# Optimization experiments

Measured on AMD Instinct MI355X. Metric: run time of the kernel, lower is better.

The kernel has to match this reference:

```python
import jax, jax.numpy as jnp
import numpy as np

Z, Y, X = 32, 480, 480          # sparse voxel grid (LiDAR-scale)
N = 200_000                     # active voxels
C_IN, C_OUT = 64, 64
EPS = 1e-5


def _subm_conv(f, nbr, w):
    """Submanifold sparse conv as gather-matmul-accumulate.
    f: [N, Cin]; nbr: [N, K] neighbor row ids, pad index == N for missing;
    w: [K, Cin, Cout]."""
    f_pad = jnp.concatenate([f, jnp.zeros((1, f.shape[1]), f.dtype)], axis=0)
    g = f_pad[nbr]                       # [N, K, Cin] gathered neighbor features
    return jnp.einsum('nkc,kco->no', g, w)


def _bn(x, gamma, beta):
    # BatchNorm1d in training mode: batch stats over the N dimension
    m = x.mean(axis=0)
    v = x.var(axis=0)
    return (x - m) * jax.lax.rsqrt(v + EPS) * gamma + beta


def setup_inputs() -> dict:
    rng = np.random.default_rng(0)
    ids = rng.choice(Z * Y * X, size=N, replace=False)
    lookup = np.full(Z * Y * X, -1, dtype=np.int64)
    lookup[ids] = np.arange(N)
    z = ids // (Y * X)
    y = (ids // X) % Y
    x = ids % X

    def nbr_table(offsets):
        cols = []
        for dz, dy, dx in offsets:
            zz, yy, xx = z + dz, y + dy, x + dx
            ok = (zz >= 0) & (zz < Z) & (yy >= 0) & (yy < Y) & (xx >= 0) & (xx < X)
            lin = np.clip((zz * Y + yy) * X + xx, 0, Z * Y * X - 1)
            idx = np.where(ok, lookup[lin], -1)
            cols.append(np.where(idx >= 0, idx, N))   # pad index N -> zero row
        return jnp.asarray(np.stack(cols, axis=1).astype(np.int32))

    off13 = [(0, dy, dx) for dy in (-1, 0, 1) for dx in (-1, 0, 1)]  # kernel (1,3,3)
    off31 = [(dz, 0, dx) for dz in (-1, 0, 1) for dx in (-1, 0, 1)]  # kernel (3,1,3)

    key = jax.random.key(0)
    ks = jax.random.split(key, 5)
    s = 0.05
    ones = jnp.ones((C_OUT,), jnp.float32)
    zeros = jnp.zeros((C_OUT,), jnp.float32)
    return {
        'features': jax.random.normal(ks[0], (N, C_IN), jnp.float32),
        'w1':   jax.random.normal(ks[1], (9, C_IN, C_OUT), jnp.float32) * s,
        'w1_2': jax.random.normal(ks[2], (9, C_OUT, C_OUT), jnp.float32) * s,
        'w2':   jax.random.normal(ks[3], (9, C_IN, C_OUT), jnp.float32) * s,
        'w3':   jax.random.normal(ks[4], (9, C_OUT, C_OUT), jnp.float32) * s,
        'g0': ones, 'b0': zeros, 'g0_2': ones, 'b0_2': zeros,
        'g1': ones, 'b1': zeros, 'g2': ones, 'b2': zeros,
        'nbr13': nbr_table(off13),
        'nbr31': nbr_table(off31),
    }


def reference(features, w1, w1_2, w2, w3, g0, b0, g0_2, b0_2, g1, b1, g2, b2,
              nbr13, nbr31):
    # shortcut branch: conv1x3 -> LeakyReLU -> BN -> conv3x1 -> LeakyReLU -> BN
    sc = _subm_conv(features, nbr13, w1)
    sc = _bn(jax.nn.leaky_relu(sc), g0, b0)
    sc = _subm_conv(sc, nbr31, w1_2)
    sc = _bn(jax.nn.leaky_relu(sc), g0_2, b0_2)
    # main branch: conv3x1 -> LeakyReLU -> BN -> conv1x3 -> LeakyReLU -> BN
    r = _subm_conv(features, nbr31, w2)
    r = _bn(jax.nn.leaky_relu(r), g1, b1)
    r = _subm_conv(r, nbr13, w3)
    r = _bn(jax.nn.leaky_relu(r), g2, b2)
    return r + sc
```

## Files before the change

### kernel.cpp

```cpp
#include <hip/hip_runtime.h>

#define NVOX 200000
#define TM 128
#define NBLK 1563
#define NBLK3 521
#define NREP 32
#define STG 4224

typedef unsigned short u16;
typedef unsigned int u32;
typedef __bf16 bf16x8 __attribute__((ext_vector_type(8)));
typedef float f32x16 __attribute__((ext_vector_type(16)));

__device__ __forceinline__ float bf2f(u16 h) { return __uint_as_float(((u32)h) << 16); }
__device__ __forceinline__ u16 f2bf(float x) {
  u32 u = __float_as_uint(x);
  u32 r = u + 0x7fffu + ((u >> 16) & 1u);
  return (u16)(r >> 16);
}
__device__ __forceinline__ uint4 cvt8(uint4 a, uint4 b) {
  const float* fa = (const float*)&a;
  const float* fb = (const float*)&b;
  uint4 r;
  u16* q = (u16*)&r;
#pragma unroll
  for (int j = 0; j < 4; ++j) { q[j] = f2bf(fa[j]); q[4 + j] = f2bf(fb[j]); }
  return r;
}

template <int PHASE>
__global__ __launch_bounds__(256, 2)
void conv_fused(const u16* __restrict__ inA, const u16* __restrict__ inB,
                const int* __restrict__ nbrA, const int* __restrict__ nbrB,
                const u16* __restrict__ wfA, const u16* __restrict__ wfB,
                const u16* __restrict__ zrow,
                void* yA, void* yB, float* __restrict__ stA, float* __restrict__ stB) {
  __shared__ float sred[4][128];

  const int tid = threadIdx.x;
  const int bid = blockIdx.x;
  const bool hB = (bid >= NBLK3);
  const int blk = hB ? bid - NBLK3 : bid;
  const u16* f = hB ? inB : inA;
  const int* nbr = hB ? nbrB : nbrA;
  const u16* wf = hB ? wfB : wfA;
  float* st = hB ? stB : stA;

  const int wv = tid >> 6;
  const int lane = tid & 63;
  const int lrow = lane & 31;
  const int lq = lane >> 5;
  const int wbase = blk * 384 + wv * 96;
  const int gr0 = wbase + lrow;
  const int gr1 = gr0 + 32;
  const int gr2 = gr0 + 64;

  constexpr bool FOLDED = (PHASE == 1);
  constexpr int KSTRIDE = FOLDED ? 5120 : 4096;

  f32x16 zz = {0.f, 0.f, 0.f, 0.f, 0.f, 0.f, 0.f, 0.f,
               0.f, 0.f, 0.f, 0.f, 0.f, 0.f, 0.f, 0.f};
  f32x16 a00 = zz, a01 = zz, a10 = zz, a11 = zz, a20 = zz, a21 = zz;

  int ic0 = (gr0 < NVOX) ? nbr[gr0 * 9] : NVOX;
  int ic1 = (gr1 < NVOX) ? nbr[gr1 * 9] : NVOX;
  int ic2 = (gr2 < NVOX) ? nbr[gr2 * 9] : NVOX;

  uint4 X[4], Y[4];

  for (int k = 0; k < 9; ++k) {
    const u16* wb = wf + k * KSTRIDE;
    bf16x8 wreg[8];
#pragma unroll
    for (int fi = 0; fi < 8; ++fi)
      wreg[fi] = __builtin_bit_cast(bf16x8, *(const uint4*)(wb + fi * 512 + lane * 8));
    bf16x8 wrb0, wrb1;
    if constexpr (FOLDED) {
      wrb0 = __builtin_bit_cast(bf16x8, *(const uint4*)(wb + 8 * 512 + lane * 8));
      wrb1 = __builtin_bit_cast(bf16x8, *(const uint4*)(wb + 9 * 512 + lane * 8));
    }
    int in0 = NVOX, in1 = NVOX, in2 = NVOX;
    if (k < 8) {
      in0 = (gr0 < NVOX) ? nbr[gr0 * 9 + k + 1] : NVOX;
      in1 = (gr1 < NVOX) ? nbr[gr1 * 9 + k + 1] : NVOX;
      in2 = (gr2 < NVOX) ? nbr[gr2 * 9 + k + 1] : NVOX;
    }

    const bool l0 = (k == 4) || (__ballot(ic0 < NVOX) != 0ull);
    const bool l1 = (k == 4) || (__ballot(ic1 < NVOX) != 0ull);
    const bool l2 = (k == 4) || (__ballot(ic2 < NVOX) != 0ull);

    auto G = [&](uint4 (&d)[4], int id) {
      const u16* p = (id < NVOX) ? (f + (size_t)id * 64) : zrow;
      p += lq * 8;
      d[0] = *(const uint4*)(p);
      d[1] = *(const uint4*)(p + 16);
      d[2] = *(const uint4*)(p + 32);
      d[3] = *(const uint4*)(p + 48);
    };
    auto MMA = [&](f32x16& c0, f32x16& c1, const uint4 (&s)[4], int id) {
#pragma unroll
      for (int ksi = 0; ksi < 4; ++ksi) {
        bf16x8 a = __builtin_bit_cast(bf16x8, s[ksi]);
        c0 = __builtin_amdgcn_mfma_f32_32x32x16_bf16(a, wreg[ksi * 2], c0, 0, 0, 0);
        c1 = __builtin_amdgcn_mfma_f32_32x32x16_bf16(a, wreg[ksi * 2 + 1], c1, 0, 0, 0);
      }
      if constexpr (FOLDED) {
        uint4 a4 = make_uint4(0u, 0u, 0u, 0u);
        if (lq == 0 && id < NVOX) ((u16*)&a4)[0] = 0x3F80u;
        bf16x8 a = __builtin_bit_cast(bf16x8, a4);
        c0 = __builtin_amdgcn_mfma_f32_32x32x16_bf16(a, wrb0, c0, 0, 0, 0);
        c1 = __builtin_amdgcn_mfma_f32_32x32x16_bf16(a, wrb1, c1, 0, 0, 0);
      }
    };

    if (l0) G(X, ic0);
    if (l1) G(Y, ic1);
    if (l0) MMA(a00, a01, X, ic0);
    if (l2) G(X, ic2);
    if (l1) MMA(a10, a11, Y, ic1);
    if (l2) MMA(a20, a21, X, ic2);

    ic0 = in0; ic1 = in1; ic2 = in2;
  }

  const bool f32out = (PHASE == 1) && !hB;
  float* yf = (float*)yA;
  u16* yb = (u16*)(hB ? yB : yA);
  float s0 = 0.f, q0 = 0.f, s1 = 0.f, q1 = 0.f;

  auto EPI = [&](const f32x16& c0, const f32x16& c1, int g) {
    const int row0 = wbase + g * 32 + 4 * lq;
#pragma unroll
    for (int r = 0; r < 16; ++r) {
      float v = c0[r]; v = v > 0.f ? v : 0.01f * v;
      float w = c1[r]; w = w > 0.f ? w : 0.01f * w;
      s0 += v; q0 += v * v; s1 += w; q1 += w * w;
      const int row = row0 + (r & 3) + 8 * (r >> 2);
      if (row < NVOX) {
        if (f32out) {
          yf[(size_t)row * 64 + lrow] = v;
          yf[(size_t)row * 64 + 32 + lrow] = w;
        } else {
          yb[(size_t)row * 64 + lrow] = f2bf(v);
          yb[(size_t)row * 64 + 32 + lrow] = f2bf(w);
        }
      }
    }
  };
  EPI(a00, a01, 0); EPI(a10, a11, 1); EPI(a20, a21, 2);

  s0 += __shfl_xor(s0, 32); q0 += __shfl_xor(q0, 32);
  s1 += __shfl_xor(s1, 32); q1 += __shfl_xor(q1, 32);
  if (lq == 0) {
    sred[wv][lrow] = s0; sred[wv][32 + lrow] = s1;
    sred[wv][64 + lrow] = q0; sred[wv][96 + lrow] = q1;
  }
  __syncthreads();
  if (tid < 128) {
    int which = tid >> 6, c = tid & 63;
    float v = sred[0][which * 64 + c] + sred[1][which * 64 + c] +
              sred[2][which * 64 + c] + sred[3][which * 64 + c];
    atomicAdd(&st[(bid & (NREP - 1)) * 128 + which * 64 + c], v);
  }
}

template <bool IN_F32, bool FOLDED, int MODE>
__global__ __launch_bounds__(256, 4)
void conv_k(const void* __restrict__ fv, const int* __restrict__ nbr,
            const u16* __restrict__ wf, void* yv, float* __restrict__ st,
            float* io, const float* __restrict__ affD,
            const float* __restrict__ affB) {
  __shared__ __align__(16) float fb[128 * 68];
  __shared__ float sred[4][128];

  const int tid = threadIdx.x;
  const int wv = tid >> 6;
  const int lane = tid & 63;
  const int lrow = lane & 31;
  const int lq = lane >> 5;
  const int base = blockIdx.x * TM;
  const int gr = base + wv * 32 + lrow;

  int ids[9];
#pragma unroll
  for (int j = 0; j < 9; ++j) ids[j] = (gr < NVOX) ? nbr[gr * 9 + j] : NVOX;

  f32x16 acc0 = {0.f, 0.f, 0.f, 0.f, 0.f, 0.f, 0.f, 0.f,
                 0.f, 0.f, 0.f, 0.f, 0.f, 0.f, 0.f, 0.f};
  f32x16 acc1 = acc0;
  constexpr int KSTRIDE = FOLDED ? 5120 : 4096;

#pragma unroll
  for (int k = 0; k < 9; ++k) {
    if (k != 4) {
      if (__ballot(ids[k] < NVOX) == 0ull) continue;
    }
    const int id = ids[k];
    const bool ok = id < NVOX;
    uint4 af[4];
    if constexpr (IN_F32) {
      const float* p = (const float*)fv + (size_t)id * 64 + lq * 8;
#pragma unroll
      for (int ksi = 0; ksi < 4; ++ksi) {
        uint4 v0 = make_uint4(0u, 0u, 0u, 0u), v1 = v0;
        if (ok) { v0 = *(const uint4*)(p + ksi * 16); v1 = *(const uint4*)(p + ksi * 16 + 4); }
        af[ksi] = cvt8(v0, v1);
      }
    } else {
      const u16* p = (const u16*)fv + (size_t)id * 64 + lq * 8;
#pragma unroll
      for (int ksi = 0; ksi < 4; ++ksi) {
        uint4 v = make_uint4(0u, 0u, 0u, 0u);
        if (ok) v = *(const uint4*)(p + ksi * 16);
        af[ksi] = v;
      }
    }
    const u16* wb = wf + k * KSTRIDE;
#pragma unroll
    for (int ksi = 0; ksi < 4; ++ksi) {
      bf16x8 a = __builtin_bit_cast(bf16x8, af[ksi]);
      bf16x8 b0 = __builtin_bit_cast(bf16x8, *(const uint4*)(wb + (ksi * 2) * 512 + lane * 8));
      bf16x8 b1 = __builtin_bit_cast(bf16x8, *(const uint4*)(wb + (ksi * 2 + 1) * 512 + lane * 8));
      acc0 = __builtin_amdgcn_mfma_f32_32x32x16_bf16(a, b0, acc0, 0, 0, 0);
      acc1 = __builtin_amdgcn_mfma_f32_32x32x16_bf16(a, b1, acc1, 0, 0, 0);
    }
    if constexpr (FOLDED) {
      uint4 a4 = make_uint4(0u, 0u, 0u, 0u);
      if (lq == 0 && ok) ((u16*)&a4)[0] = 0x3F80u;
      bf16x8 a = __builtin_bit_cast(bf16x8, a4);
      bf16x8 b0 = __builtin_bit_cast(bf16x8, *(const uint4*)(wb + 8 * 512 + lane * 8));
      bf16x8 b1 = __builtin_bit_cast(bf16x8, *(const uint4*)(wb + 9 * 512 + lane * 8));
      acc0 = __builtin_amdgcn_mfma_f32_32x32x16_bf16(a, b0, acc0, 0, 0, 0);
      acc1 = __builtin_amdgcn_mfma_f32_32x32x16_bf16(a, b1, acc1, 0, 0, 0);
    }
  }

  const int cc0 = lrow, cc1 = 32 + lrow;
  float aD0 = 0.f, aD1 = 0.f, hD0 = 0.f, hD1 = 0.f;
  if constexpr (MODE == 2) {
    aD0 = affD[cc0]; hD0 = affD[64 + cc0];
    aD1 = affD[cc1]; hD1 = affD[64 + cc1];
  }
  float s0 = 0.f, q0 = 0.f, s1 = 0.f, q1 = 0.f;
  float vout[2][16];
#pragma unroll
  for (int r = 0; r < 16; ++r) {
    float v = acc0[r]; v = v > 0.f ? v : 0.01f * v;
    s0 += v; q0 += v * v; vout[0][r] = v;
    float w = acc1[r]; w = w > 0.f ? w : 0.01f * w;
    s1 += w; q1 += w * w; vout[1][r] = w;
  }
  if constexpr (MODE != 2) {
    s0 += __shfl_xor(s0, 32); q0 += __shfl_xor(q0, 32);
    s1 += __shfl_xor(s1, 32); q1 += __shfl_xor(q1, 32);
    if (lq == 0) {
      sred[wv][lrow] = s0; sred[wv][32 + lrow] = s1;
      sred[wv][64 + lrow] = q0; sred[wv][96 + lrow] = q1;
    }
  }
  if constexpr (MODE == 0) {
    u16* bb = (u16*)fb;
#pragma unroll
    for (int r = 0; r < 16; ++r) {
      int rowD = 32 * wv + (r & 3) + 8 * (r >> 2) + 4 * lq;
      bb[rowD * 72 + cc0] = f2bf(vout[0][r]);
      bb[rowD * 72 + cc1] = f2bf(vout[1][r]);
    }
  } else if constexpr (MODE == 2 || MODE == 3) {
#pragma unroll
    for (int r = 0; r < 16; ++r) {
      int rowD = 32 * wv + (r & 3) + 8 * (r >> 2) + 4 * lq;
      float v0 = vout[0][r], v1 = vout[1][r];
      if constexpr (MODE == 2) { v0 = fmaf(v0, aD0, hD0); v1 = fmaf(v1, aD1, hD1); }
      fb[rowD * 68 + cc0] = v0;
      fb[rowD * 68 + cc1] = v1;
    }
  }
  __syncthreads();

  const int trow = tid >> 3, cp = tid & 7;
  if constexpr (MODE == 0) {
    u16* y = (u16*)yv;
    const u16* bb = (const u16*)fb;
#pragma unroll
    for (int it = 0; it < 4; ++it) {
      int r = it * 32 + trow, row = base + r;
      if (row < NVOX)
        *(uint4*)(y + (size_t)row * 64 + cp * 8) = *(const uint4*)(bb + r * 72 + cp * 8);
    }
  }
  if constexpr (MODE == 3) {
    float* y = (float*)yv;
#pragma unroll
    for (int it = 0; it < 4; ++it) {
      int r = it * 32 + trow, row = base + r;
      if (row < NVOX) {
        *(float4*)(y + (size_t)row * 64 + cp * 8) = *(const float4*)(fb + r * 68 + cp * 8);
        *(float4*)(y + (size_t)row * 64 + cp * 8 + 4) = *(const float4*)(fb + r * 68 + cp * 8 + 4);
      }
    }
  }
  if constexpr (MODE == 2) {
    float* y = (float*)yv;
#pragma unroll
    for (int it = 0; it < 4; ++it) {
      int r = it * 32 + trow, row = base + r;
      if (row < NVOX) {
        float t[8], p[8], o[8];
        *(float4*)&t[0] = *(const float4*)(fb + r * 68 + cp * 8);
        *(float4*)&t[4] = *(const float4*)(fb + r * 68 + cp * 8 + 4);
        *(float4*)&p[0] = *(const float4*)(io + (size_t)row * 64 + cp * 8);
        *(float4*)&p[4] = *(const float4*)(io + (size_t)row * 64 + cp * 8 + 4);
#pragma unroll
        for (int j = 0; j < 8; ++j) {
          int c = cp * 8 + j;
          o[j] = t[j] + fmaf(p[j], affB[c], affB[64 + c]);
        }
        *(float4*)(y + (size_t)row * 64 + cp * 8) = *(const float4*)&o[0];
        *(float4*)(y + (size_t)row * 64 + cp * 8 + 4) = *(const float4*)&o[4];
      }
    }
  }
  if constexpr (MODE != 2) {
    if (tid < 128) {
      int which = tid >> 6, c = tid & 63;
      float v = sred[0][which * 64 + c] + sred[1][which * 64 + c] +
                sred[2][which * 64 + c] + sred[3][which * 64 + c];
      atomicAdd(&st[(blockIdx.x & (NREP - 1)) * 128 + which * 64 + c], v);
    }
  }
}

__global__ void prep_all(const float* __restrict__ feat, const float* __restrict__ w1,
                         const float* __restrict__ w2, u16* __restrict__ wf,
                         u16* __restrict__ F, float* __restrict__ st,
                         u16* __restrict__ zr, int cvt_blocks) {
  const int bid = blockIdx.x, tid = threadIdx.x;
  if (bid < cvt_blocks) {
    int i8 = (bid * 256 + tid) * 8;
    if (i8 < NVOX * 64) {
      uint4 a = *(const uint4*)(feat + i8);
      uint4 b = *(const uint4*)(feat + i8 + 4);
      *(uint4*)(F + i8) = cvt8(a, b);
    }
    return;
  }
  int rb = bid - cvt_blocks;
  if (rb < 288) {
    int e = rb * 256 + tid;
    int slot = e / 36864, r = e % 36864;
    int k = r >> 12, rr = r & 4095;
    int frag = rr >> 9, lane = (rr >> 3) & 63, j = rr & 7;
    int ks = frag >> 1, ct = frag & 1;
    int cin = ks * 16 + (lane >> 5) * 8 + j;
    int cout = ct * 32 + (lane & 31);
    const float* src = slot ? w2 : w1;
    wf[e] = f2bf(src[k * 4096 + cin * 64 + cout]);
    return;
  }
  for (int i = tid; i < 4 * STG; i += 256) st[i] = 0.f;
  if (tid < 32) ((u32*)zr)[tid] = 0u;
}

__device__ __forceinline__ void bn_from_replicas(const float* stp, const float* g,
                                                 const float* b, int c,
                                                 float* sc, float* sh) {
  float s = 0.f, q = 0.f;
#pragma unroll
  for (int r = 0; r < NREP; ++r) {
    s += stp[r * 128 + c];
    q += stp[r * 128 + 64 + c];
  }
  const float invn = 1.0f / (float)NVOX;
  float mean = s * invn;
  float var = q * invn - mean * mean;
  float sca = g[c] * rsqrtf(var + 1e-5f);
  *sc = sca;
  *sh = b[c] - mean * sca;
}

__global__ void wscale2(const float* __restrict__ wA, float* __restrict__ stpA,
                        const float* __restrict__ gA, const float* __restrict__ bA,
                        u16* __restrict__ dA,
                        const float* __restrict__ wB, float* __restrict__ stpB,
                        const float* __restrict__ gB, const float* __restrict__ bB,
                        u16* __restrict__ dB) {
  __shared__ float sc[64], sh[64];
  const int tid = threadIdx.x;
  const bool hB = (blockIdx.x >= 180);
  const float* wraw = hB ? wB : wA;
  float* stp = hB ? stpB : stpA;
  const float* g = hB ? gB : gA;
  const float* b = hB ? bB : bA;
  u16* dst = hB ? dB : dA;
  const int blk = hB ? blockIdx.x - 180 : blockIdx.x;
  if (tid < 64) {
    float a, h;
    bn_from_replicas(stp, g, b, tid, &a, &h);
    sc[tid] = a; sh[tid] = h;
    if (blk == 0) { stp[NREP * 128 + tid] = a; stp[NREP * 128 + 64 + tid] = h; }
  }
  __syncthreads();
  int e = blk * 256 + tid;
  int k = e / 5120, r = e % 5120;
  int frag = r >> 9, lane = (r >> 3) & 63, j = r & 7;
  int ks = frag >> 1, ct = frag & 1;
  int cout = ct * 32 + (lane & 31);
  u16 val = 0;
  if (ks < 4) {
    int cin = ks * 16 + (lane >> 5) * 8 + j;
    val = f2bf(sc[cin] * wraw[k * 4096 + cin * 64 + cout]);
  } else if (((lane >> 5) == 0) && j == 0) {
    float acc = 0.f;
    for (int c = 0; c < 64; ++c) acc += sh[c] * wraw[k * 4096 + c * 64 + cout];
    val = f2bf(acc);
  }
  dst[e] = val;
}

__global__ void finalize2(float* __restrict__ stA, const float* __restrict__ gA,
                          const float* __restrict__ bA, float* __restrict__ stB,
                          const float* __restrict__ gB, const float* __restrict__ bB) {
  int t = threadIdx.x;
  float* stp = (t < 64) ? stA : stB;
  const float* g = (t < 64) ? gA : gB;
  const float* b = (t < 64) ? bA : bB;
  int c = t & 63;
  if (t < 128) {
    float a, h;
    bn_from_replicas(stp, g, b, c, &a, &h);
    stp[NREP * 128 + c] = a;
    stp[NREP * 128 + 64 + c] = h;
  }
}

__global__ void final_add(const u16* __restrict__ y3, float* io,
                          const float* __restrict__ affB, const float* __restrict__ affD) {
  int i8 = (blockIdx.x * 256 + threadIdx.x) * 8;
  if (i8 < NVOX * 64) {
    float a[8];
    *(float4*)&a[0] = *(const float4*)(io + i8);
    *(float4*)&a[4] = *(const float4*)(io + i8 + 4);
    uint4 vd = *(const uint4*)(y3 + i8);
    const u16* pd = (const u16*)&vd;
    int cb = i8 & 63;
    float o[8];
#pragma unroll
    for (int j = 0; j < 8; ++j) {
      int c = cb + j;
      o[j] = fmaf(a[j], affB[c], affB[64 + c]) + fmaf(bf2f(pd[j]), affD[c], affD[64 + c]);
    }
    *(float4*)(io + i8) = *(const float4*)&o[0];
    *(float4*)(io + i8 + 4) = *(const float4*)&o[4];
  }
}

extern "C" void kernel_launch(void* const* d_in, const int* in_sizes, int n_in,
                              void* d_out, int out_size, void* d_ws, size_t ws_size,
                              hipStream_t stream) {
  const float* feat = (const float*)d_in[0];
  const float* w1 = (const float*)d_in[1];
  const float* w1_2 = (const float*)d_in[2];
  const float* w2 = (const float*)d_in[3];
  const float* w3 = (const float*)d_in[4];
  const float* g0 = (const float*)d_in[5];
  const float* b0 = (const float*)d_in[6];
  const float* g0_2 = (const float*)d_in[7];
  const float* b0_2 = (const float*)d_in[8];
  const float* g1 = (const float*)d_in[9];
  const float* b1 = (const float*)d_in[10];
  const float* g2 = (const float*)d_in[11];
  const float* b2 = (const float*)d_in[12];
  const int* nbr13 = (const int*)d_in[13];
  const int* nbr31 = (const int*)d_in[14];
  float* out = (float*)d_out;

  char* ws = (char*)d_ws;
  float* st = (float*)ws;
  u16* wf = (u16*)(ws + 67584);
  u16* s0 = wf;
  u16* s1 = wf + 36864;
  u16* s2 = wf + 73728;
  u16* s3 = wf + 119808;
  u16* zr = (u16*)(ws + 399360);
  u16* F = (u16*)(ws + 399488);
  u16* A1 = F + (size_t)NVOX * 64;
  u16* A2 = A1 + (size_t)NVOX * 64;
  const size_t base_sz = 399488;
  const size_t need_fused = base_sz + 3ull * NVOX * 64 * 2;
  const size_t need_serial = base_sz + 2ull * NVOX * 64 * 2;

  float* st0 = st, *st1 = st + STG, *st2 = st + 2 * STG, *st3 = st + 3 * STG;

  if (ws_size >= need_fused) {
    prep_all<<<6539, 256, 0, stream>>>(feat, w1, w2, wf, F, st, zr, 6250);
    conv_fused<0><<<2 * NBLK3, 256, 0, stream>>>(F, F, nbr13, nbr31, s0, s1, zr,
                                                 A1, A2, st0, st2);
    wscale2<<<360, 256, 0, stream>>>(w1_2, st0, g0, b0, s2, w3, st2, g1, b1, s3);
    conv_fused<1><<<2 * NBLK3, 256, 0, stream>>>(A1, A2, nbr31, nbr13, s2, s3, zr,
                                                 out, F, st1, st3);
    finalize2<<<1, 128, 0, stream>>>(st1, g0_2, b0_2, st3, g2, b2);
    final_add<<<6250, 256, 0, stream>>>(F, out, st1 + NREP * 128, st3 + NREP * 128);
  } else if (ws_size >= need_serial) {
    prep_all<<<6539, 256, 0, stream>>>(feat, w1, w2, wf, F, st, zr, 6250);
    conv_k<false, false, 0><<<NBLK, 256, 0, stream>>>(F, nbr13, s0, A1, st0, nullptr, nullptr, nullptr);
    wscale2<<<180, 256, 0, stream>>>(w1_2, st0, g0, b0, s2, w3, st2, g1, b1, s3);
    conv_k<false, true, 3><<<NBLK, 256, 0, stream>>>(A1, nbr31, s2, out, st1, nullptr, nullptr, nullptr);
    conv_k<false, false, 0><<<NBLK, 256, 0, stream>>>(F, nbr31, s1, A1, st2, nullptr, nullptr, nullptr);
    wscale2<<<360, 256, 0, stream>>>(w1_2, st0, g0, b0, s2, w3, st2, g1, b1, s3);
    conv_k<false, true, 0><<<NBLK, 256, 0, stream>>>(A1, nbr13, s3, F, st3, nullptr, nullptr, nullptr);
    finalize2<<<1, 128, 0, stream>>>(st1, g0_2, b0_2, st3, g2, b2);
    final_add<<<6250, 256, 0, stream>>>(F, out, st1 + NREP * 128, st3 + NREP * 128);
  } else {
    u16* Az = F;
    prep_all<<<289, 256, 0, stream>>>(feat, w1, w2, wf, nullptr, st, zr, 0);
    conv_k<true, false, 0><<<NBLK, 256, 0, stream>>>(feat, nbr13, s0, Az, st0, nullptr, nullptr, nullptr);
    wscale2<<<180, 256, 0, stream>>>(w1_2, st0, g0, b0, s2, w3, st2, g1, b1, s3);
    conv_k<false, true, 3><<<NBLK, 256, 0, stream>>>(Az, nbr31, s2, out, st1, nullptr, nullptr, nullptr);
    finalize2<<<1, 128, 0, stream>>>(st1, g0_2, b0_2, st3, g2, b2);
    conv_k<true, false, 0><<<NBLK, 256, 0, stream>>>(feat, nbr31, s1, Az, st2, nullptr, nullptr, nullptr);
    wscale2<<<360, 256, 0, stream>>>(w1_2, st0, g0, b0, s2, w3, st2, g1, b1, s3);
    conv_k<false, true, 1><<<NBLK, 256, 0, stream>>>(Az, nbr13, s3, nullptr, st3, nullptr, nullptr, nullptr);
    finalize2<<<1, 128, 0, stream>>>(st1, g0_2, b0_2, st3, g2, b2);
    conv_k<false, true, 2><<<NBLK, 256, 0, stream>>>(Az, nbr13, s3, out, nullptr, out,
                                                     st3 + NREP * 128, st1 + NREP * 128);
  }
}
```

Measured before the change: 271.1 us.

## Rebalance conv work to two-row-group passes, raise occupancy, fuse BN finalize

Each wave now processes row groups in passes of two (plus one or two single-group passes) instead of three at once. This lowers register pressure so the launch bound can allow four blocks per CU. The grid becomes exactly 512 blocks per branch, and the leftover groups go to a permuted subset of waves, so the row bounds checks are dropped. The separate BN finalize kernel is folded into the final add kernel, which computes the affine parameters in shared memory per block. The trade-offs are uneven work across waves and the BN stats being recomputed by every block.

```diff
diff --git a/kernel.cpp b/kernel.cpp
--- a/kernel.cpp
+++ b/kernel.cpp
@@ -3,7 +3,7 @@
 #define NVOX 200000
 #define TM 128
 #define NBLK 1563
-#define NBLK3 521
+#define BPS 512
 #define NREP 32
 #define STG 4224
 
@@ -29,7 +29,7 @@
 }
 
 template <int PHASE>
-__global__ __launch_bounds__(256, 2)
+__global__ __launch_bounds__(256, 4)
 void conv_fused(const u16* __restrict__ inA, const u16* __restrict__ inB,
                 const int* __restrict__ nbrA, const int* __restrict__ nbrB,
                 const u16* __restrict__ wfA, const u16* __restrict__ wfB,
@@ -39,8 +39,8 @@
 
   const int tid = threadIdx.x;
   const int bid = blockIdx.x;
-  const bool hB = (bid >= NBLK3);
-  const int blk = hB ? bid - NBLK3 : bid;
+  const bool hB = (bid >= BPS);
+  const int blk = hB ? bid - BPS : bid;
   const u16* f = hB ? inB : inA;
   const int* nbr = hB ? nbrB : nbrA;
   const u16* wf = hB ? wfB : wfA;
@@ -50,105 +50,92 @@
   const int lane = tid & 63;
   const int lrow = lane & 31;
   const int lq = lane >> 5;
-  const int wbase = blk * 384 + wv * 96;
-  const int gr0 = wbase + lrow;
-  const int gr1 = gr0 + 32;
-  const int gr2 = gr0 + 64;
+  const int W = blk * 4 + wv;
 
   constexpr bool FOLDED = (PHASE == 1);
   constexpr int KSTRIDE = FOLDED ? 5120 : 4096;
-
-  f32x16 zz = {0.f, 0.f, 0.f, 0.f, 0.f, 0.f, 0.f, 0.f,
-               0.f, 0.f, 0.f, 0.f, 0.f, 0.f, 0.f, 0.f};
-  f32x16 a00 = zz, a01 = zz, a10 = zz, a11 = zz, a20 = zz, a21 = zz;
-
-  int ic0 = (gr0 < NVOX) ? nbr[gr0 * 9] : NVOX;
-  int ic1 = (gr1 < NVOX) ? nbr[gr1 * 9] : NVOX;
-  int ic2 = (gr2 < NVOX) ? nbr[gr2 * 9] : NVOX;
-
-  uint4 X[4], Y[4];
-
-  for (int k = 0; k < 9; ++k) {
-    const u16* wb = wf + k * KSTRIDE;
-    bf16x8 wreg[8];
-#pragma unroll
-    for (int fi = 0; fi < 8; ++fi)
-      wreg[fi] = __builtin_bit_cast(bf16x8, *(const uint4*)(wb + fi * 512 + lane * 8));
-    bf16x8 wrb0, wrb1;
-    if constexpr (FOLDED) {
-      wrb0 = __builtin_bit_cast(bf16x8, *(const uint4*)(wb + 8 * 512 + lane * 8));
-      wrb1 = __builtin_bit_cast(bf16x8, *(const uint4*)(wb + 9 * 512 + lane * 8));
-    }
-    int in0 = NVOX, in1 = NVOX, in2 = NVOX;
-    if (k < 8) {
-      in0 = (gr0 < NVOX) ? nbr[gr0 * 9 + k + 1] : NVOX;
-      in1 = (gr1 < NVOX) ? nbr[gr1 * 9 + k + 1] : NVOX;
-      in2 = (gr2 < NVOX) ? nbr[gr2 * 9 + k + 1] : NVOX;
-    }
-
-    const bool l0 = (k == 4) || (__ballot(ic0 < NVOX) != 0ull);
-    const bool l1 = (k == 4) || (__ballot(ic1 < NVOX) != 0ull);
-    const bool l2 = (k == 4) || (__ballot(ic2 < NVOX) != 0ull);
-
-    auto G = [&](uint4 (&d)[4], int id) {
-      const u16* p = (id < NVOX) ? (f + (size_t)id * 64) : zrow;
-      p += lq * 8;
-      d[0] = *(const uint4*)(p);
-      d[1] = *(const uint4*)(p + 16);
-      d[2] = *(const uint4*)(p + 32);
-      d[3] = *(const uint4*)(p + 48);
-    };
-    auto MMA = [&](f32x16& c0, f32x16& c1, const uint4 (&s)[4], int id) {
-#pragma unroll
-      for (int ksi = 0; ksi < 4; ++ksi) {
-        bf16x8 a = __builtin_bit_cast(bf16x8, s[ksi]);
-        c0 = __builtin_amdgcn_mfma_f32_32x32x16_bf16(a, wreg[ksi * 2], c0, 0, 0, 0);
-        c1 = __builtin_amdgcn_mfma_f32_32x32x16_bf16(a, wreg[ksi * 2 + 1], c1, 0, 0, 0);
-      }
-      if constexpr (FOLDED) {
-        uint4 a4 = make_uint4(0u, 0u, 0u, 0u);
-        if (lq == 0 && id < NVOX) ((u16*)&a4)[0] = 0x3F80u;
-        bf16x8 a = __builtin_bit_cast(bf16x8, a4);
-        c0 = __builtin_amdgcn_mfma_f32_32x32x16_bf16(a, wrb0, c0, 0, 0, 0);
-        c1 = __builtin_amdgcn_mfma_f32_32x32x16_bf16(a, wrb1, c1, 0, 0, 0);
-      }
-    };
-
-    if (l0) G(X, ic0);
-    if (l1) G(Y, ic1);
-    if (l0) MMA(a00, a01, X, ic0);
-    if (l2) G(X, ic2);
-    if (l1) MMA(a10, a11, Y, ic1);
-    if (l2) MMA(a20, a21, X, ic2);
-
-    ic0 = in0; ic1 = in1; ic2 = in2;
-  }
-
   const bool f32out = (PHASE == 1) && !hB;
   float* yf = (float*)yA;
   u16* yb = (u16*)(hB ? yB : yA);
+
   float s0 = 0.f, q0 = 0.f, s1 = 0.f, q1 = 0.f;
 
+  auto G = [&](uint4 (&d)[4], int id) {
+    const u16* p = (id < NVOX) ? (f + (size_t)id * 64) : zrow;
+    p += lq * 8;
+    d[0] = *(const uint4*)(p);
+    d[1] = *(const uint4*)(p + 16);
+    d[2] = *(const uint4*)(p + 32);
+    d[3] = *(const uint4*)(p + 48);
+  };
+  auto MMA = [&](f32x16& c0, f32x16& c1, const uint4 (&s)[4], int id,
+                 const bf16x8* wr, const u16* wb) {
+#pragma unroll
+    for (int ksi = 0; ksi < 4; ++ksi) {
+      bf16x8 a = __builtin_bit_cast(bf16x8, s[ksi]);
+      c0 = __builtin_amdgcn_mfma_f32_32x32x16_bf16(a, wr[ksi * 2], c0, 0, 0, 0);
+      c1 = __builtin_amdgcn_mfma_f32_32x32x16_bf16(a, wr[ksi * 2 + 1], c1, 0, 0, 0);
+    }
+    if constexpr (FOLDED) {
+      uint4 a4 = make_uint4(0u, 0u, 0u, 0u);
+      if (lq == 0 && id < NVOX) ((u16*)&a4)[0] = 0x3F80u;
+      bf16x8 a = __builtin_bit_cast(bf16x8, a4);
+      bf16x8 b0 = __builtin_bit_cast(bf16x8, *(const uint4*)(wb + 8 * 512 + lane * 8));
+      bf16x8 b1 = __builtin_bit_cast(bf16x8, *(const uint4*)(wb + 9 * 512 + lane * 8));
+      c0 = __builtin_amdgcn_mfma_f32_32x32x16_bf16(a, b0, c0, 0, 0, 0);
+      c1 = __builtin_amdgcn_mfma_f32_32x32x16_bf16(a, b1, c1, 0, 0, 0);
+    }
+  };
   auto EPI = [&](const f32x16& c0, const f32x16& c1, int g) {
-    const int row0 = wbase + g * 32 + 4 * lq;
+    const int row0 = g * 32 + 4 * lq;
 #pragma unroll
     for (int r = 0; r < 16; ++r) {
       float v = c0[r]; v = v > 0.f ? v : 0.01f * v;
       float w = c1[r]; w = w > 0.f ? w : 0.01f * w;
       s0 += v; q0 += v * v; s1 += w; q1 += w * w;
       const int row = row0 + (r & 3) + 8 * (r >> 2);
-      if (row < NVOX) {
-        if (f32out) {
-          yf[(size_t)row * 64 + lrow] = v;
-          yf[(size_t)row * 64 + 32 + lrow] = w;
-        } else {
-          yb[(size_t)row * 64 + lrow] = f2bf(v);
-          yb[(size_t)row * 64 + 32 + lrow] = f2bf(w);
-        }
+      if (f32out) {
+        yf[(size_t)row * 64 + lrow] = v;
+        yf[(size_t)row * 64 + 32 + lrow] = w;
+      } else {
+        yb[(size_t)row * 64 + lrow] = f2bf(v);
+        yb[(size_t)row * 64 + 32 + lrow] = f2bf(w);
       }
     }
   };
-  EPI(a00, a01, 0); EPI(a10, a11, 1); EPI(a20, a21, 2);
+
+  const f32x16 zz = {0.f, 0.f, 0.f, 0.f, 0.f, 0.f, 0.f, 0.f,
+                     0.f, 0.f, 0.f, 0.f, 0.f, 0.f, 0.f, 0.f};
+
+  auto PASS = [&](int gA, int gB, bool two) {
+    f32x16 c00 = zz, c01 = zz, c10 = zz, c11 = zz;
+    const int grA = gA * 32 + lrow;
+    const int grB = gB * 32 + lrow;
+    int icA = nbr[grA * 9];
+    int icB = two ? nbr[grB * 9] : NVOX;
+    uint4 X[4];
+    for (int k = 0; k < 9; ++k) {
+      const u16* wb = wf + k * KSTRIDE;
+      bf16x8 wreg[8];
+#pragma unroll
+      for (int fi = 0; fi < 8; ++fi)
+        wreg[fi] = __builtin_bit_cast(bf16x8, *(const uint4*)(wb + fi * 512 + lane * 8));
+      int inA = (k < 8) ? nbr[grA * 9 + k + 1] : NVOX;
+      int inB = (two && k < 8) ? nbr[grB * 9 + k + 1] : NVOX;
+      const bool lA = (k == 4) || (__ballot(icA < NVOX) != 0ull);
+      const bool lB = two && ((k == 4) || (__ballot(icB < NVOX) != 0ull));
+      if (lA) { G(X, icA); MMA(c00, c01, X, icA, wreg, wb); }
+      if (lB) { G(X, icB); MMA(c10, c11, X, icB, wreg, wb); }
+      icA = inA; icB = inB;
+    }
+    EPI(c00, c01, gA);
+    if (two) EPI(c10, c11, gB);
+  };
+
+  PASS(2 * W, 2 * W + 1, true);
+  PASS(4096 + W, 0, false);
+  const int P = (W * 1321) & 2047;
+  if (P < 106) PASS(6144 + P, 0, false);
 
   s0 += __shfl_xor(s0, 32); q0 += __shfl_xor(q0, 32);
   s1 += __shfl_xor(s1, 32); q1 += __shfl_xor(q1, 32);
@@ -456,6 +443,38 @@
   }
 }
 
+__global__ void final_add2(const u16* __restrict__ y3, float* io,
+                           float* __restrict__ stB, const float* __restrict__ gB,
+                           const float* __restrict__ bB,
+                           float* __restrict__ stD, const float* __restrict__ gD,
+                           const float* __restrict__ bD) {
+  __shared__ float aff[4][64];
+  const int t = threadIdx.x;
+  if (t < 128) {
+    float a, h;
+    if (t < 64) { bn_from_replicas(stB, gB, bB, t, &a, &h); aff[0][t] = a; aff[1][t] = h; }
+    else { int c = t - 64; bn_from_replicas(stD, gD, bD, c, &a, &h); aff[2][c] = a; aff[3][c] = h; }
+  }
+  __syncthreads();
+  int i8 = (blockIdx.x * 256 + t) * 8;
+  if (i8 < NVOX * 64) {
+    float a[8];
+    *(float4*)&a[0] = *(const float4*)(io + i8);
+    *(float4*)&a[4] = *(const float4*)(io + i8 + 4);
+    uint4 vd = *(const uint4*)(y3 + i8);
+    const u16* pd = (const u16*)&vd;
+    int cb = i8 & 63;
+    float o[8];
+#pragma unroll
+    for (int j = 0; j < 8; ++j) {
+      int c = cb + j;
+      o[j] = fmaf(a[j], aff[0][c], aff[1][c]) + fmaf(bf2f(pd[j]), aff[2][c], aff[3][c]);
+    }
+    *(float4*)(io + i8) = *(const float4*)&o[0];
+    *(float4*)(io + i8 + 4) = *(const float4*)&o[4];
+  }
+}
+
 extern "C" void kernel_launch(void* const* d_in, const int* in_sizes, int n_in,
                               void* d_out, int out_size, void* d_ws, size_t ws_size,
                               hipStream_t stream) {
@@ -495,13 +514,12 @@
 
   if (ws_size >= need_fused) {
     prep_all<<<6539, 256, 0, stream>>>(feat, w1, w2, wf, F, st, zr, 6250);
-    conv_fused<0><<<2 * NBLK3, 256, 0, stream>>>(F, F, nbr13, nbr31, s0, s1, zr,
-                                                 A1, A2, st0, st2);
+    conv_fused<0><<<2 * BPS, 256, 0, stream>>>(F, F, nbr13, nbr31, s0, s1, zr,
+                                               A1, A2, st0, st2);
     wscale2<<<360, 256, 0, stream>>>(w1_2, st0, g0, b0, s2, w3, st2, g1, b1, s3);
-    conv_fused<1><<<2 * NBLK3, 256, 0, stream>>>(A1, A2, nbr31, nbr13, s2, s3, zr,
-                                                 out, F, st1, st3);
-    finalize2<<<1, 128, 0, stream>>>(st1, g0_2, b0_2, st3, g2, b2);
-    final_add<<<6250, 256, 0, stream>>>(F, out, st1 + NREP * 128, st3 + NREP * 128);
+    conv_fused<1><<<2 * BPS, 256, 0, stream>>>(A1, A2, nbr31, nbr13, s2, s3, zr,
+                                               out, F, st1, st3);
+    final_add2<<<6250, 256, 0, stream>>>(F, out, st1, g0_2, b0_2, st3, g2, b2);
   } else if (ws_size >= need_serial) {
     prep_all<<<6539, 256, 0, stream>>>(feat, w1, w2, wf, F, st, zr, 6250);
     conv_k<false, false, 0><<<NBLK, 256, 0, stream>>>(F, nbr13, s0, A1, st0, nullptr, nullptr, nullptr);
```

Measured after the change: 686.8 us. +153.4%, slower.
